# Kernel tuning notes

Hardware: AMD Instinct MI355X
Metric: run time of the kernel (lower is better)

The kernel has to match this reference:

```python
import jax, jax.numpy as jnp
import numpy as np


def fwht(x):
    """Fast Walsh-Hadamard transform over last axis (power-of-2 length), normalized by 1/sqrt(n).
    Matches matmul_hadU with K=1 (pure Hadamard rotation)."""
    orig_shape = x.shape
    n = orig_shape[-1]
    x = x.reshape(-1, n)
    h = 1
    while h < n:
        x = x.reshape(-1, n // (2 * h), 2, h)
        a = x[:, :, 0, :]
        b = x[:, :, 1, :]
        x = jnp.stack([a + b, a - b], axis=2)
        h *= 2
    x = x.reshape(orig_shape)
    return x * (1.0 / np.sqrt(n)).astype(np.float32)


def setup_inputs() -> dict:
    key = jax.random.key(0)
    k1, k2, k3, k4, k5 = jax.random.split(key, 5)
    B, S, n, m = 2, 2048, 4096, 4096
    CODEBOOK = 65536  # 2^16 E8P codes, each decoding an 8-dim lattice point
    inp = jax.random.normal(k1, (B, S, n), dtype=jnp.float32)
    # SU/SV are random sign-like diagonal rescales in QuIP; use unit-variance floats here
    SU = jax.random.normal(k2, (n,), dtype=jnp.float32)
    SV = jax.random.normal(k3, (m,), dtype=jnp.float32)
    grid = jax.random.normal(k4, (CODEBOOK, 8), dtype=jnp.float32) * 0.1
    Qidxs = jax.random.randint(k5, (m, n // 8), 0, CODEBOOK, dtype=jnp.int32)
    return {"input": inp, "SU": SU, "SV": SV, "grid": grid, "Qidxs": Qidxs}


def reference(input, SU, SV, grid, Qidxs):
    n = SU.shape[0]
    m = SV.shape[0]
    x = input.reshape(-1, n) * SU          # diagonal rescale by SU
    x = fwht(x)                             # left Hadamard rotation
    # Dequantize packed E8P codebook: each 16-bit code -> 8 weights
    W = grid[Qidxs].reshape(m, n)           # [m, n]
    x = x @ W.T                             # dense GEMM against dequantized weight
    x = fwht(x)                             # right Hadamard rotation
    x = x * SV                              # diagonal rescale by SV
    return x.reshape(input.shape[:-1] + (m,))
```

## Files before the change

### kernel.cpp

```cpp
#include <hip/hip_runtime.h>
#include <stdint.h>

typedef __bf16 bf16x8 __attribute__((ext_vector_type(8)));
typedef float f32x4 __attribute__((ext_vector_type(4)));

__device__ __forceinline__ unsigned int f2bf(float f) {
  unsigned int u = __float_as_uint(f);
  return (u + 0x7fffu + ((u >> 16) & 1u)) >> 16;
}
__device__ __forceinline__ unsigned int pack2(float a, float b) {
  return f2bf(a) | (f2bf(b) << 16);
}

__device__ __forceinline__ void fwht16(float v[16]) {
#pragma unroll
  for (int s = 0; s < 4; ++s) {
    const int h = 1 << s;
#pragma unroll
    for (int i = 0; i < 16; ++i) {
      if (!(i & h)) {
        float a = v[i], b = v[i ^ h];
        v[i] = a + b;
        v[i ^ h] = a - b;
      }
    }
  }
}

#define LP(i) ((i) + ((i) >> 5))

__global__ void __launch_bounds__(256) k_fwht_in(const float* __restrict__ X,
                                                 const float* __restrict__ SU,
                                                 unsigned short* __restrict__ Xh) {
  __shared__ float lds[4224];
  const int t = threadIdx.x;
  const size_t row = blockIdx.x;
  const float4* xr = (const float4*)(X + row * 4096);
  const float4* su = (const float4*)SU;
  float v[16];
#pragma unroll
  for (int q = 0; q < 4; ++q) {
    float4 a = xr[4 * t + q], s = su[4 * t + q];
    v[4 * q + 0] = a.x * s.x;
    v[4 * q + 1] = a.y * s.y;
    v[4 * q + 2] = a.z * s.z;
    v[4 * q + 3] = a.w * s.w;
  }
  fwht16(v);
#pragma unroll
  for (int q = 0; q < 4; ++q) {
    int i0 = 16 * t + 4 * q;
    *(float4*)&lds[LP(i0)] = make_float4(v[4 * q], v[4 * q + 1], v[4 * q + 2], v[4 * q + 3]);
  }
  __syncthreads();
  const int b = ((t >> 4) << 8) | (t & 15);
#pragma unroll
  for (int j = 0; j < 16; ++j) { int i = b + 16 * j; v[j] = lds[LP(i)]; }
  fwht16(v);
#pragma unroll
  for (int j = 0; j < 16; ++j) { int i = b + 16 * j; lds[LP(i)] = v[j]; }
  __syncthreads();
#pragma unroll
  for (int j = 0; j < 16; ++j) { int i = t + 256 * j; v[j] = lds[LP(i)]; }
  fwht16(v);
  unsigned short* orow = Xh + row * 4096;
#pragma unroll
  for (int j = 0; j < 16; ++j)
    orow[t + 256 * j] = (unsigned short)f2bf(v[j] * 0.015625f);
}

__global__ void __launch_bounds__(256) k_decompress(const int* __restrict__ Qidxs,
                                                    const float* __restrict__ G,
                                                    unsigned short* __restrict__ Wh) {
  int e = blockIdx.x * 256 + threadIdx.x;
  int idx = Qidxs[e];
  const float4* g = (const float4*)(G + (size_t)idx * 8);
  float4 a = g[0], b = g[1];
  uint4 o;
  o.x = pack2(a.x, a.y);
  o.y = pack2(a.z, a.w);
  o.z = pack2(b.x, b.y);
  o.w = pack2(b.z, b.w);
  ((uint4*)Wh)[e] = o;
}

__device__ __forceinline__ void gl2lds16(const unsigned short* g, unsigned short* l) {
  __builtin_amdgcn_global_load_lds(
      (const __attribute__((address_space(1))) void*)g,
      (__attribute__((address_space(3))) void*)l, 16, 0, 0);
}

__global__ void __launch_bounds__(256) k_gemm_bt(const unsigned short* __restrict__ A,
                                                 const unsigned short* __restrict__ B,
                                                 float* __restrict__ C) {
  const int K = 4096, N = 4096;
  __shared__ unsigned short sA[128 * 64];
  __shared__ unsigned short sB[128 * 64];
  const int tid = threadIdx.x;
  const int wave = tid >> 6, lane = tid & 63;
  const int bn = blockIdx.x, bm = blockIdx.y;
  const int wr = wave >> 1, wc = wave & 1;
  const int frow = lane & 15;
  const int sw = frow & 7;
  const int jbase = lane >> 4;
  f32x4 acc[4][4] = {};

  const size_t rowA0 = (size_t)bm * 128;
  const size_t rowB0 = (size_t)bn * 128;

  for (int kt = 0; kt < K; kt += 64) {
    __syncthreads();
#pragma unroll
    for (int it = 0; it < 4; ++it) {
      int c = it * 256 + tid;
      int r = c >> 3;
      int jg = (c & 7) ^ (r & 7);
      int kc = jg * 8;
      unsigned short* la = &sA[(it * 256 + wave * 64) * 8];
      unsigned short* lb = &sB[(it * 256 + wave * 64) * 8];
      gl2lds16(A + (rowA0 + r) * K + kt + kc, la);
      gl2lds16(B + (rowB0 + r) * K + kt + kc, lb);
    }
    __syncthreads();
#pragma unroll
    for (int kk = 0; kk < 64; kk += 32) {
      bf16x8 af[4], bfr[4];
      int jn = (kk >> 3) + jbase;
      int js = jn ^ sw;
#pragma unroll
      for (int i = 0; i < 4; ++i)
        af[i] = *(const bf16x8*)&sA[(wr * 64 + i * 16 + frow) * 64 + js * 8];
#pragma unroll
      for (int j = 0; j < 4; ++j)
        bfr[j] = *(const bf16x8*)&sB[(wc * 64 + j * 16 + frow) * 64 + js * 8];
#pragma unroll
      for (int i = 0; i < 4; ++i)
#pragma unroll
        for (int j = 0; j < 4; ++j)
          acc[i][j] = __builtin_amdgcn_mfma_f32_16x16x32_bf16(af[i], bfr[j], acc[i][j], 0, 0, 0);
    }
  }
  const int crow = bm * 128 + wr * 64 + (lane >> 4) * 4;
  const int ccol = bn * 128 + wc * 64 + (lane & 15);
#pragma unroll
  for (int i = 0; i < 4; ++i)
#pragma unroll
    for (int j = 0; j < 4; ++j) {
      float* cp = C + (size_t)(crow + i * 16) * N + ccol + j * 16;
#pragma unroll
      for (int r = 0; r < 4; ++r) cp[(size_t)r * N] = acc[i][j][r];
    }
}

__global__ void __launch_bounds__(256) k_fwht_out(float* __restrict__ Y,
                                                  const float* __restrict__ SV) {
  __shared__ float lds[4224];
  const int t = threadIdx.x;
  const size_t row = blockIdx.x;
  float* yrow = Y + row * 4096;
  const float4* yr = (const float4*)yrow;
  float v[16];
#pragma unroll
  for (int q = 0; q < 4; ++q) {
    float4 a = yr[4 * t + q];
    v[4 * q + 0] = a.x;
    v[4 * q + 1] = a.y;
    v[4 * q + 2] = a.z;
    v[4 * q + 3] = a.w;
  }
  fwht16(v);
#pragma unroll
  for (int q = 0; q < 4; ++q) {
    int i0 = 16 * t + 4 * q;
    *(float4*)&lds[LP(i0)] = make_float4(v[4 * q], v[4 * q + 1], v[4 * q + 2], v[4 * q + 3]);
  }
  __syncthreads();
  const int b = ((t >> 4) << 8) | (t & 15);
#pragma unroll
  for (int j = 0; j < 16; ++j) { int i = b + 16 * j; v[j] = lds[LP(i)]; }
  fwht16(v);
#pragma unroll
  for (int j = 0; j < 16; ++j) { int i = b + 16 * j; lds[LP(i)] = v[j]; }
  __syncthreads();
#pragma unroll
  for (int j = 0; j < 16; ++j) { int i = t + 256 * j; v[j] = lds[LP(i)]; }
  fwht16(v);
#pragma unroll
  for (int j = 0; j < 16; ++j) {
    int i = t + 256 * j;
    yrow[i] = v[j] * SV[i] * 0.015625f;
  }
}

extern "C" void kernel_launch(void* const* d_in, const int* in_sizes, int n_in,
                              void* d_out, int out_size, void* d_ws, size_t ws_size,
                              hipStream_t stream) {
  const float* X     = (const float*)d_in[0];
  const float* SU    = (const float*)d_in[1];
  const float* SV    = (const float*)d_in[2];
  const float* G     = (const float*)d_in[3];
  const int*   Qidxs = (const int*)d_in[4];
  float* out = (float*)d_out;

  unsigned short* Xh = (unsigned short*)d_ws;
  unsigned short* Wh = Xh + (size_t)4096 * 4096;

  k_fwht_in<<<4096, 256, 0, stream>>>(X, SU, Xh);
  k_decompress<<<(4096 * 512) / 256, 256, 0, stream>>>(Qidxs, G, Wh);
  k_gemm_bt<<<dim3(32, 32), 256, 0, stream>>>(Xh, Wh, out);
  k_fwht_out<<<4096, 256, 0, stream>>>(out, SV);
}
```

Baseline: 317.7 us.

## Fold both Hadamard rotations into dequantized weight and fuse SV into GEMM epilogue

Moves the input and output Hadamard transforms from the activations onto the dequantized weight: rows are transformed with SU folded in, and columns via two 64-point strided passes. Activations are only cast to bf16, and SV scaling is applied in the GEMM epilogue. This removes the separate fp32 output Hadamard pass over the result. It adds extra bf16 rounding steps on the weight and strided column passes.

```diff
diff --git a/kernel.cpp b/kernel.cpp
--- a/kernel.cpp
+++ b/kernel.cpp
@@ -29,59 +29,82 @@
 
 #define LP(i) ((i) + ((i) >> 5))
 
-__global__ void __launch_bounds__(256) k_fwht_in(const float* __restrict__ X,
-                                                 const float* __restrict__ SU,
-                                                 unsigned short* __restrict__ Xh) {
-  __shared__ float lds[4224];
-  const int t = threadIdx.x;
-  const size_t row = blockIdx.x;
-  const float4* xr = (const float4*)(X + row * 4096);
-  const float4* su = (const float4*)SU;
-  float v[16];
-#pragma unroll
-  for (int q = 0; q < 4; ++q) {
-    float4 a = xr[4 * t + q], s = su[4 * t + q];
-    v[4 * q + 0] = a.x * s.x;
-    v[4 * q + 1] = a.y * s.y;
-    v[4 * q + 2] = a.z * s.z;
-    v[4 * q + 3] = a.w * s.w;
-  }
-  fwht16(v);
-#pragma unroll
-  for (int q = 0; q < 4; ++q) {
-    int i0 = 16 * t + 4 * q;
-    *(float4*)&lds[LP(i0)] = make_float4(v[4 * q], v[4 * q + 1], v[4 * q + 2], v[4 * q + 3]);
-  }
-  __syncthreads();
-  const int b = ((t >> 4) << 8) | (t & 15);
-#pragma unroll
-  for (int j = 0; j < 16; ++j) { int i = b + 16 * j; v[j] = lds[LP(i)]; }
-  fwht16(v);
-#pragma unroll
-  for (int j = 0; j < 16; ++j) { int i = b + 16 * j; lds[LP(i)] = v[j]; }
-  __syncthreads();
-#pragma unroll
-  for (int j = 0; j < 16; ++j) { int i = t + 256 * j; v[j] = lds[LP(i)]; }
-  fwht16(v);
-  unsigned short* orow = Xh + row * 4096;
-#pragma unroll
-  for (int j = 0; j < 16; ++j)
-    orow[t + 256 * j] = (unsigned short)f2bf(v[j] * 0.015625f);
-}
-
-__global__ void __launch_bounds__(256) k_decompress(const int* __restrict__ Qidxs,
-                                                    const float* __restrict__ G,
-                                                    unsigned short* __restrict__ Wh) {
-  int e = blockIdx.x * 256 + threadIdx.x;
-  int idx = Qidxs[e];
-  const float4* g = (const float4*)(G + (size_t)idx * 8);
-  float4 a = g[0], b = g[1];
+__global__ void __launch_bounds__(256) k_cast(const float* __restrict__ X,
+                                              unsigned short* __restrict__ Xb) {
+  size_t i = (size_t)blockIdx.x * 2048 + (size_t)threadIdx.x * 8;
+  float4 a = *(const float4*)(X + i);
+  float4 b = *(const float4*)(X + i + 4);
   uint4 o;
   o.x = pack2(a.x, a.y);
   o.y = pack2(a.z, a.w);
   o.z = pack2(b.x, b.y);
   o.w = pack2(b.z, b.w);
-  ((uint4*)Wh)[e] = o;
+  *(uint4*)(Xb + i) = o;
+}
+
+__global__ void __launch_bounds__(256) k_wrow(const int* __restrict__ Qidxs,
+                                              const float* __restrict__ G,
+                                              const float* __restrict__ SU,
+                                              unsigned short* __restrict__ W) {
+  __shared__ float lds[4224];
+  const int t = threadIdx.x;
+  const size_t m = blockIdx.x;
+  int2 code = ((const int2*)(Qidxs + m * 512))[t];
+  const float4* g0 = (const float4*)(G + (size_t)code.x * 8);
+  const float4* g1 = (const float4*)(G + (size_t)code.y * 8);
+  float4 c0 = g0[0], c1 = g0[1], c2 = g1[0], c3 = g1[1];
+  float v[16] = {c0.x, c0.y, c0.z, c0.w, c1.x, c1.y, c1.z, c1.w,
+                 c2.x, c2.y, c2.z, c2.w, c3.x, c3.y, c3.z, c3.w};
+  fwht16(v);
+#pragma unroll
+  for (int q = 0; q < 4; ++q) {
+    int i0 = 16 * t + 4 * q;
+    *(float4*)&lds[LP(i0)] = make_float4(v[4 * q], v[4 * q + 1], v[4 * q + 2], v[4 * q + 3]);
+  }
+  __syncthreads();
+  const int b = ((t >> 4) << 8) | (t & 15);
+#pragma unroll
+  for (int j = 0; j < 16; ++j) { int i = b + 16 * j; v[j] = lds[LP(i)]; }
+  fwht16(v);
+#pragma unroll
+  for (int j = 0; j < 16; ++j) { int i = b + 16 * j; lds[LP(i)] = v[j]; }
+  __syncthreads();
+#pragma unroll
+  for (int j = 0; j < 16; ++j) { int i = t + 256 * j; v[j] = lds[LP(i)]; }
+  fwht16(v);
+  unsigned short* orow = W + m * 4096;
+#pragma unroll
+  for (int j = 0; j < 16; ++j) {
+    int i = t + 256 * j;
+    orow[i] = (unsigned short)f2bf(v[j] * SU[i] * 0.015625f);
+  }
+}
+
+__global__ void __launch_bounds__(256) k_wm(unsigned short* __restrict__ W,
+                                            int base_per_group, int rstride) {
+  const int col = blockIdx.x * 256 + threadIdx.x;
+  const int base = blockIdx.y * base_per_group + col;
+  float v[64];
+#pragma unroll
+  for (int r = 0; r < 64; ++r) {
+    unsigned int u = W[base + r * rstride];
+    v[r] = __uint_as_float(u << 16);
+  }
+#pragma unroll
+  for (int s = 0; s < 6; ++s) {
+    const int h = 1 << s;
+#pragma unroll
+    for (int i = 0; i < 64; ++i) {
+      if (!(i & h)) {
+        float a = v[i], b = v[i ^ h];
+        v[i] = a + b;
+        v[i ^ h] = a - b;
+      }
+    }
+  }
+#pragma unroll
+  for (int r = 0; r < 64; ++r)
+    W[base + r * rstride] = (unsigned short)f2bf(v[r]);
 }
 
 __device__ __forceinline__ void gl2lds16(const unsigned short* g, unsigned short* l) {
@@ -92,6 +115,7 @@
 
 __global__ void __launch_bounds__(256) k_gemm_bt(const unsigned short* __restrict__ A,
                                                  const unsigned short* __restrict__ B,
+                                                 const float* __restrict__ SV,
                                                  float* __restrict__ C) {
   const int K = 4096, N = 4096;
   __shared__ unsigned short sA[128 * 64];
@@ -142,54 +166,17 @@
   }
   const int crow = bm * 128 + wr * 64 + (lane >> 4) * 4;
   const int ccol = bn * 128 + wc * 64 + (lane & 15);
+  float sv[4];
+#pragma unroll
+  for (int j = 0; j < 4; ++j) sv[j] = SV[ccol + 16 * j] * 0.015625f;
 #pragma unroll
   for (int i = 0; i < 4; ++i)
 #pragma unroll
     for (int j = 0; j < 4; ++j) {
       float* cp = C + (size_t)(crow + i * 16) * N + ccol + j * 16;
 #pragma unroll
-      for (int r = 0; r < 4; ++r) cp[(size_t)r * N] = acc[i][j][r];
-    }
-}
-
-__global__ void __launch_bounds__(256) k_fwht_out(float* __restrict__ Y,
-                                                  const float* __restrict__ SV) {
-  __shared__ float lds[4224];
-  const int t = threadIdx.x;
-  const size_t row = blockIdx.x;
-  float* yrow = Y + row * 4096;
-  const float4* yr = (const float4*)yrow;
-  float v[16];
-#pragma unroll
-  for (int q = 0; q < 4; ++q) {
-    float4 a = yr[4 * t + q];
-    v[4 * q + 0] = a.x;
-    v[4 * q + 1] = a.y;
-    v[4 * q + 2] = a.z;
-    v[4 * q + 3] = a.w;
-  }
-  fwht16(v);
-#pragma unroll
-  for (int q = 0; q < 4; ++q) {
-    int i0 = 16 * t + 4 * q;
-    *(float4*)&lds[LP(i0)] = make_float4(v[4 * q], v[4 * q + 1], v[4 * q + 2], v[4 * q + 3]);
-  }
-  __syncthreads();
-  const int b = ((t >> 4) << 8) | (t & 15);
-#pragma unroll
-  for (int j = 0; j < 16; ++j) { int i = b + 16 * j; v[j] = lds[LP(i)]; }
-  fwht16(v);
-#pragma unroll
-  for (int j = 0; j < 16; ++j) { int i = b + 16 * j; lds[LP(i)] = v[j]; }
-  __syncthreads();
-#pragma unroll
-  for (int j = 0; j < 16; ++j) { int i = t + 256 * j; v[j] = lds[LP(i)]; }
-  fwht16(v);
-#pragma unroll
-  for (int j = 0; j < 16; ++j) {
-    int i = t + 256 * j;
-    yrow[i] = v[j] * SV[i] * 0.015625f;
-  }
+      for (int r = 0; r < 4; ++r) cp[(size_t)r * N] = acc[i][j][r] * sv[j];
+    }
 }
 
 extern "C" void kernel_launch(void* const* d_in, const int* in_sizes, int n_in,
@@ -202,11 +189,12 @@
   const int*   Qidxs = (const int*)d_in[4];
   float* out = (float*)d_out;
 
-  unsigned short* Xh = (unsigned short*)d_ws;
-  unsigned short* Wh = Xh + (size_t)4096 * 4096;
-
-  k_fwht_in<<<4096, 256, 0, stream>>>(X, SU, Xh);
-  k_decompress<<<(4096 * 512) / 256, 256, 0, stream>>>(Qidxs, G, Wh);
-  k_gemm_bt<<<dim3(32, 32), 256, 0, stream>>>(Xh, Wh, out);
-  k_fwht_out<<<4096, 256, 0, stream>>>(out, SV);
-}
+  unsigned short* Xb = (unsigned short*)d_ws;
+  unsigned short* Wh = Xb + (size_t)4096 * 4096;
+
+  k_cast<<<8192, 256, 0, stream>>>(X, Xb);
+  k_wrow<<<4096, 256, 0, stream>>>(Qidxs, G, SU, Wh);
+  k_wm<<<dim3(16, 64), 256, 0, stream>>>(Wh, 64 * 4096, 4096);
+  k_wm<<<dim3(16, 64), 256, 0, stream>>>(Wh, 4096, 64 * 4096);
+  k_gemm_bt<<<dim3(32, 32), 256, 0, stream>>>(Xb, Wh, SV, out);
+}
```

Measured after the change: 318.9 us. No clear change (+0.4%).
